# Optimization experiments

Hardware: AMD Instinct MI355X
Metric: run time of the kernel (lower is better)

The kernel has to match this reference:

```python
import jax, jax.numpy as jnp
import numpy as np

B, S, H = 2, 4096, 2048
NH, NKV, D = 16, 4, 128
BS, LOCAL, GLOB, STRIDE = 64, 8, 4, 16
SEL = GLOB + LOCAL
SCALE = D ** -0.5
NEG = -1e9


def rotate_half(x):
    x1, x2 = x[..., : D // 2], x[..., D // 2 :]
    return jnp.concatenate([-x2, x1], axis=-1)


def setup_inputs():
    key = jax.random.key(0)
    ks = jax.random.split(key, 5)
    hidden_states = jax.random.normal(ks[0], (B, S, H), dtype=jnp.float32)
    # standard RoPE tables, shape [B, S, D] as the module expects (cos.unsqueeze(1))
    pos = jnp.arange(S, dtype=jnp.float32)
    inv = 1.0 / (10000.0 ** (jnp.arange(0, D, 2, dtype=jnp.float32) / D))
    freqs = pos[:, None] * inv[None, :]
    emb = jnp.concatenate([freqs, freqs], axis=-1)
    cos = jnp.broadcast_to(jnp.cos(emb)[None], (B, S, D)).astype(jnp.float32)
    sin = jnp.broadcast_to(jnp.sin(emb)[None], (B, S, D)).astype(jnp.float32)
    std = 0.02
    Wq = jax.random.normal(ks[1], (NH * D, H), dtype=jnp.float32) * std
    Wk = jax.random.normal(ks[2], (NKV * D, H), dtype=jnp.float32) * std
    Wv = jax.random.normal(ks[3], (NKV * D, H), dtype=jnp.float32) * std
    Wo = jax.random.normal(ks[4], (H, NH * D), dtype=jnp.float32) * std
    return {"hidden_states": hidden_states, "cos": cos, "sin": sin,
            "Wq": Wq, "Wk": Wk, "Wv": Wv, "Wo": Wo}


def _block_sparse_attn(q, k, v):
    # q, k, v: [B, NH, S, D]; past_len = 0, attention_mask = None (all keys valid)
    qb = S // BS
    kb = S // BS
    qid = jnp.arange(qb)
    # local blocks: the LOCAL most recent blocks ending at the query block
    loc = qid[:, None] - (LOCAL - 1 - jnp.arange(LOCAL)[None, :])
    loc = jnp.clip(loc, 0, kb - 1)
    # global blocks: strided anchors
    g = jnp.clip(jnp.arange(GLOB) * STRIDE, 0, kb - 1)
    glob = jnp.broadcast_to(g[None, :], (qb, GLOB))
    sel = jnp.concatenate([glob, loc], axis=1)  # [qb, SEL]
    valid = sel <= qid[:, None]                 # causal at block level
    # dedup: drop a selected block if an earlier slot selected the same block
    eq = sel[:, :, None] == sel[:, None, :]
    lower = jnp.tril(jnp.ones((SEL, SEL), dtype=bool), k=-1)
    keep = (~(eq & lower[None]).any(-1)) & valid  # [qb, SEL]

    k_blk = k.reshape(B, NH, kb, BS, D)
    v_blk = v.reshape(B, NH, kb, BS, D)
    k_sel = jnp.take(k_blk, sel.reshape(-1), axis=2).reshape(B, NH, qb, SEL * BS, D)
    v_sel = jnp.take(v_blk, sel.reshape(-1), axis=2).reshape(B, NH, qb, SEL * BS, D)
    q_blk = q.reshape(B, NH, qb, BS, D)

    scores = jnp.einsum("bhqid,bhqjd->bhqij", q_blk, k_sel) * SCALE  # [B,NH,qb,BS,SEL*BS]
    keep_tok = jnp.broadcast_to(keep[:, :, None], (qb, SEL, BS)).reshape(qb, SEL * BS)
    scores = scores + (1.0 - keep_tok.astype(scores.dtype))[None, None, :, None, :] * NEG
    # intra-block causal mask where selected block == query block
    same = (sel == qid[:, None]).astype(scores.dtype)  # [qb, SEL]
    intra = jnp.triu(jnp.full((BS, BS), NEG, dtype=scores.dtype), k=1)
    scores6 = scores.reshape(B, NH, qb, BS, SEL, BS)
    scores6 = scores6 + intra[None, None, None, :, None, :] * same[None, None, :, None, :, None]
    scores = scores6.reshape(B, NH, qb, BS, SEL * BS)
    probs = jax.nn.softmax(scores, axis=-1)
    out = jnp.einsum("bhqij,bhqjd->bhqid", probs, v_sel)
    return out.reshape(B, NH, S, D)


def reference(hidden_states, cos, sin, Wq, Wk, Wv, Wo):
    q = (hidden_states @ Wq.T).reshape(B, S, NH, D).transpose(0, 2, 1, 3)
    k = (hidden_states @ Wk.T).reshape(B, S, NKV, D).transpose(0, 2, 1, 3)
    v = (hidden_states @ Wv.T).reshape(B, S, NKV, D).transpose(0, 2, 1, 3)
    c = cos[:, None, :, :]
    s = sin[:, None, :, :]
    q = q * c + rotate_half(q) * s
    k = k * c + rotate_half(k) * s
    rep = NH // NKV
    k = jnp.repeat(k, rep, axis=1)
    v = jnp.repeat(v, rep, axis=1)
    out = _block_sparse_attn(q, k, v)
    out = out.transpose(0, 2, 1, 3).reshape(B, S, NH * D)
    return out @ Wo.T
```

## Files before the change

### kernel.cpp

```cpp
#include <hip/hip_runtime.h>

typedef __bf16 bf16_t;
typedef __bf16 bf16x8_t __attribute__((ext_vector_type(8)));
typedef __bf16 bf16x4_t __attribute__((ext_vector_type(4)));
typedef float f32x4_t __attribute__((ext_vector_type(4)));
typedef unsigned short u16;
typedef unsigned int u32;

#define B_ 2
#define S_ 4096
#define NH_ 16
#define NKV_ 4
#define D_ 128
#define NEG_ (-1000000000.0f)
#define SCALE_ 0.08838834764831845f

__device__ __forceinline__ void load16(const bf16_t* g, bf16_t* l) {
  __builtin_amdgcn_global_load_lds(
      (__attribute__((address_space(1))) void*)(g),
      (__attribute__((address_space(3))) void*)(l),
      16, 0, 0);
}

__global__ __launch_bounds__(256) void cvt_kernel(const float* __restrict__ in,
                                                  bf16_t* __restrict__ out, int n4) {
  int i = blockIdx.x * 256 + threadIdx.x;
  if (i < n4) {
    float4 v = ((const float4*)in)[i];
    bf16x4_t o;
    o.x = (bf16_t)v.x; o.y = (bf16_t)v.y; o.z = (bf16_t)v.z; o.w = (bf16_t)v.w;
    *(bf16x4_t*)(out + (size_t)i * 4) = o;
  }
}

template <int BF16OUT>
__global__ __launch_bounds__(256) void gemm_bt_kernel(const bf16_t* __restrict__ A,
                                                      const bf16_t* __restrict__ Bm,
                                                      float* __restrict__ Cf,
                                                      bf16_t* __restrict__ Cb,
                                                      int M, int N, int K) {
  __shared__ bf16_t As[128 * 32];
  __shared__ bf16_t Bs[128 * 32];
  const int t = threadIdx.x;
  const int lane = t & 63;
  const int w = t >> 6;
  const int wr = w >> 1, wc = w & 1;
  const int l15 = lane & 15, l4 = lane >> 4;
  const int m0 = blockIdx.x * 128;
  const int n0 = blockIdx.y * 128;

  f32x4_t acc[4][4] = {};

  for (int k0 = 0; k0 < K; k0 += 32) {
    __syncthreads();
#pragma unroll
    for (int i = 0; i < 2; i++) {
      int f = t + 256 * i;
      int row = f >> 2, c = f & 3;
      load16(A + (size_t)(m0 + row) * K + k0 + c * 8, As + (w * 64 + i * 256) * 8);
      load16(Bm + (size_t)(n0 + row) * K + k0 + c * 8, Bs + (w * 64 + i * 256) * 8);
    }
    __syncthreads();
    bf16x8_t af[4], bfr[4];
#pragma unroll
    for (int mi = 0; mi < 4; mi++)
      af[mi] = *(const bf16x8_t*)&As[(wr * 64 + mi * 16 + l15) * 32 + l4 * 8];
#pragma unroll
    for (int ni = 0; ni < 4; ni++)
      bfr[ni] = *(const bf16x8_t*)&Bs[(wc * 64 + ni * 16 + l15) * 32 + l4 * 8];
#pragma unroll
    for (int mi = 0; mi < 4; mi++)
#pragma unroll
      for (int ni = 0; ni < 4; ni++)
        acc[mi][ni] = __builtin_amdgcn_mfma_f32_16x16x32_bf16(af[mi], bfr[ni], acc[mi][ni], 0, 0, 0);
  }

#pragma unroll
  for (int mi = 0; mi < 4; mi++)
#pragma unroll
    for (int ni = 0; ni < 4; ni++)
#pragma unroll
      for (int r = 0; r < 4; r++) {
        int grow = m0 + wr * 64 + mi * 16 + l4 * 4 + r;
        int gcol = n0 + wc * 64 + ni * 16 + l15;
        float v = acc[mi][ni][r];
        if (BF16OUT) Cb[(size_t)grow * N + gcol] = (bf16_t)v;
        else Cf[(size_t)grow * N + gcol] = v;
      }
}

__global__ __launch_bounds__(320) void rope_kernel(const bf16_t* __restrict__ qkv,
                                                   const float* __restrict__ cosp,
                                                   const float* __restrict__ sinp,
                                                   bf16_t* __restrict__ Qro,
                                                   bf16_t* __restrict__ Kro) {
  const int tk = blockIdx.x;
  const int b = tk >> 12;
  const int s = tk & 4095;
  const int sblock = s >> 6, row = s & 63;
  const int idx = threadIdx.x;
  int head, lc;
  const bf16_t* base;
  bf16_t* outp;
  if (idx < 256) {
    head = idx >> 4; lc = idx & 15;
    base = qkv + (size_t)tk * 3072 + head * 128;
    outp = Qro + ((size_t)(b * NH_ + head) * 64 + sblock) * 8192;
  } else {
    int i2 = idx - 256;
    head = i2 >> 4; lc = i2 & 15;
    base = qkv + (size_t)tk * 3072 + 2048 + head * 128;
    outp = Kro + ((size_t)(b * NKV_ + head) * 64 + sblock) * 8192;
  }
  const int d0 = lc * 8;
  bf16x8_t x = *(const bf16x8_t*)(base + d0);
  const int d0p = (d0 < 64) ? d0 + 64 : d0 - 64;
  bf16x8_t xp = *(const bf16x8_t*)(base + d0p);
  const float sgn = (d0 < 64) ? -1.0f : 1.0f;
  const float* cb = cosp + (size_t)tk * 128 + d0;
  const float* sb = sinp + (size_t)tk * 128 + d0;
  bf16x8_t o;
#pragma unroll
  for (int e = 0; e < 8; e++)
    o[e] = (bf16_t)((float)x[e] * cb[e] + sgn * (float)xp[e] * sb[e]);
  *(bf16x8_t*)(outp + (lc * 64 + row) * 8) = o;
}

__global__ __launch_bounds__(256) void vtrans_kernel(const u16* __restrict__ qkv,
                                                     u16* __restrict__ vt) {
  __shared__ u16 tile[64][136];
  const int sblock = blockIdx.x;
  const int kh = blockIdx.y;
  const int b = blockIdx.z;
  const int t = threadIdx.x;
#pragma unroll
  for (int i = 0; i < 4; i++) {
    int f = t + 256 * i;
    int sl = f >> 4, c = f & 15;
    uint4 vv = *(const uint4*)(qkv + (size_t)(b * S_ + sblock * 64 + sl) * 3072 + 2560 + kh * 128 + c * 8);
    *(uint4*)&tile[sl][c * 8] = vv;
  }
  __syncthreads();
  u16* out = vt + ((size_t)(b * NKV_ + kh) * 64 + sblock) * 8192;
#pragma unroll
  for (int i = 0; i < 4; i++) {
    int g = t + 256 * i;
    int sc = g >> 7, d = g & 127;
    u16 e0 = tile[sc * 8 + 0][d], e1 = tile[sc * 8 + 1][d];
    u16 e2 = tile[sc * 8 + 2][d], e3 = tile[sc * 8 + 3][d];
    u16 e4 = tile[sc * 8 + 4][d], e5 = tile[sc * 8 + 5][d];
    u16 e6 = tile[sc * 8 + 6][d], e7 = tile[sc * 8 + 7][d];
    uint4 ov;
    ov.x = (u32)e0 | ((u32)e1 << 16);
    ov.y = (u32)e2 | ((u32)e3 << 16);
    ov.z = (u32)e4 | ((u32)e5 << 16);
    ov.w = (u32)e6 | ((u32)e7 << 16);
    *(uint4*)(out + (size_t)g * 8) = ov;
  }
}

__global__ __launch_bounds__(256) void attn_kernel(const bf16_t* __restrict__ Qr,
                                                   const bf16_t* __restrict__ Kr,
                                                   const bf16_t* __restrict__ Vt,
                                                   bf16_t* __restrict__ Ao) {
  __shared__ bf16_t Ks[8192];
  __shared__ bf16_t Vs[8192];
  __shared__ bf16_t Ps[4 * 16 * 72];
  const int qid = blockIdx.x;
  const int h = blockIdx.y;
  const int b = blockIdx.z;
  const int kh = h >> 2;
  const int t = threadIdx.x;
  const int lane = t & 63;
  const int w = t >> 6;
  const int l15 = lane & 15, l4 = lane >> 4;

  int keep_mask = 0;
#pragma unroll
  for (int j = 0; j < 12; j++) {
    int cj;
    if (j < 4) cj = j * 16;
    else { cj = qid - 11 + j; cj = cj < 0 ? 0 : cj; cj = cj > 63 ? 63 : cj; }
    bool keep = (cj <= qid);
#pragma unroll
    for (int i = 0; i < j; i++) {
      int ci;
      if (i < 4) ci = i * 16;
      else { ci = qid - 11 + i; ci = ci < 0 ? 0 : ci; ci = ci > 63 ? 63 : ci; }
      if (ci == cj) keep = false;
    }
    if (keep) keep_mask |= (1 << j);
  }

  const bf16_t* Qg = Qr + ((size_t)(b * NH_ + h) * 64 + qid) * 8192;
  const bf16_t* Kg = Kr + ((size_t)(b * NKV_ + kh) * 64) * 8192;
  const bf16_t* Vg = Vt + ((size_t)(b * NKV_ + kh) * 64) * 8192;

#pragma unroll
  for (int i = 0; i < 4; i++) {
    int f = t + 256 * i;
    load16(Qg + (size_t)f * 8, Ks + (w * 64 + i * 256) * 8);
  }
  __syncthreads();
  bf16x8_t qa[4];
#pragma unroll
  for (int ks = 0; ks < 4; ks++)
    qa[ks] = *(const bf16x8_t*)&Ks[((ks * 4 + l4) * 64 + w * 16 + l15) * 8];

  float mi_r[4], li_r[4];
  f32x4_t oacc[8] = {};
#pragma unroll
  for (int r = 0; r < 4; r++) { mi_r[r] = -__builtin_inff(); li_r[r] = 0.0f; }

#pragma unroll 1
  for (int j = 0; j < 12; j++) {
    if (!(keep_mask & (1 << j))) continue;
    int cj;
    if (j < 4) cj = j * 16;
    else { cj = qid - 11 + j; cj = cj < 0 ? 0 : cj; cj = cj > 63 ? 63 : cj; }

    __syncthreads();
#pragma unroll
    for (int i = 0; i < 4; i++) {
      int f = t + 256 * i;
      load16(Kg + (size_t)cj * 8192 + (size_t)f * 8, Ks + (w * 64 + i * 256) * 8);
      load16(Vg + (size_t)cj * 8192 + (size_t)f * 8, Vs + (w * 64 + i * 256) * 8);
    }
    __syncthreads();

    f32x4_t sacc[4] = {};
#pragma unroll
    for (int ks = 0; ks < 4; ks++) {
#pragma unroll
      for (int ni = 0; ni < 4; ni++) {
        bf16x8_t kb = *(const bf16x8_t*)&Ks[((ks * 4 + l4) * 64 + ni * 16 + l15) * 8];
        sacc[ni] = __builtin_amdgcn_mfma_f32_16x16x32_bf16(qa[ks], kb, sacc[ni], 0, 0, 0);
      }
    }

    const bool diag = (cj == qid);
    float sv[4][4];
#pragma unroll
    for (int ni = 0; ni < 4; ni++)
#pragma unroll
      for (int r = 0; r < 4; r++) {
        float x = sacc[ni][r] * SCALE_;
        if (diag && (ni * 16 + l15) > (w * 16 + l4 * 4 + r)) x += NEG_;
        sv[ni][r] = x;
      }

    float rmax[4], rsum[4], alpha[4], p[4][4];
#pragma unroll
    for (int r = 0; r < 4; r++)
      rmax[r] = fmaxf(fmaxf(sv[0][r], sv[1][r]), fmaxf(sv[2][r], sv[3][r]));
#pragma unroll
    for (int msk = 1; msk < 16; msk <<= 1)
#pragma unroll
      for (int r = 0; r < 4; r++)
        rmax[r] = fmaxf(rmax[r], __shfl_xor(rmax[r], msk, 64));
#pragma unroll
    for (int r = 0; r < 4; r++) {
      float nm = fmaxf(mi_r[r], rmax[r]);
      alpha[r] = __expf(mi_r[r] - nm);
      mi_r[r] = nm;
    }
#pragma unroll
    for (int ni = 0; ni < 4; ni++)
#pragma unroll
      for (int r = 0; r < 4; r++)
        p[ni][r] = __expf(sv[ni][r] - mi_r[r]);
#pragma unroll
    for (int r = 0; r < 4; r++)
      rsum[r] = (p[0][r] + p[1][r]) + (p[2][r] + p[3][r]);
#pragma unroll
    for (int msk = 1; msk < 16; msk <<= 1)
#pragma unroll
      for (int r = 0; r < 4; r++)
        rsum[r] += __shfl_xor(rsum[r], msk, 64);
#pragma unroll
    for (int r = 0; r < 4; r++)
      li_r[r] = li_r[r] * alpha[r] + rsum[r];
#pragma unroll
    for (int n2 = 0; n2 < 8; n2++)
#pragma unroll
      for (int r = 0; r < 4; r++)
        oacc[n2][r] *= alpha[r];

#pragma unroll
    for (int ni = 0; ni < 4; ni++)
#pragma unroll
      for (int r = 0; r < 4; r++)
        Ps[w * 1152 + (l4 * 4 + r) * 72 + ni * 16 + l15] = (bf16_t)p[ni][r];

#pragma unroll
    for (int kst = 0; kst < 2; kst++) {
      bf16x8_t pa = *(const bf16x8_t*)&Ps[w * 1152 + l15 * 72 + kst * 32 + l4 * 8];
#pragma unroll
      for (int n2 = 0; n2 < 8; n2++) {
        bf16x8_t vb = *(const bf16x8_t*)&Vs[((kst * 4 + l4) * 128 + n2 * 16 + l15) * 8];
        oacc[n2] = __builtin_amdgcn_mfma_f32_16x16x32_bf16(pa, vb, oacc[n2], 0, 0, 0);
      }
    }
  }

  float invl[4];
#pragma unroll
  for (int r = 0; r < 4; r++) invl[r] = 1.0f / li_r[r];
#pragma unroll
  for (int n2 = 0; n2 < 8; n2++)
#pragma unroll
    for (int r = 0; r < 4; r++) {
      int m = w * 16 + l4 * 4 + r;
      size_t idx = ((size_t)(b * S_ + qid * 64 + m)) * (NH_ * D_) + h * D_ + n2 * 16 + l15;
      Ao[idx] = (bf16_t)(oacc[n2][r] * invl[r]);
    }
}

extern "C" void kernel_launch(void* const* d_in, const int* in_sizes, int n_in,
                              void* d_out, int out_size, void* d_ws, size_t ws_size,
                              hipStream_t stream) {
  const float* hs = (const float*)d_in[0];
  const float* cosp = (const float*)d_in[1];
  const float* sinp = (const float*)d_in[2];
  const float* Wq = (const float*)d_in[3];
  const float* Wk = (const float*)d_in[4];
  const float* Wv = (const float*)d_in[5];
  const float* Wo = (const float*)d_in[6];
  float* outp = (float*)d_out;

  char* ws = (char*)d_ws;
  bf16_t* Xb   = (bf16_t*)(ws);
  bf16_t* Wb   = (bf16_t*)(ws + 33554432);
  bf16_t* Wob  = (bf16_t*)(ws + 46137344);
  bf16_t* QKVo = (bf16_t*)(ws + 54525952);
  bf16_t* Qr   = (bf16_t*)(ws + 104857600);
  bf16_t* Kr   = (bf16_t*)(ws + 138412032);
  bf16_t* Vt   = (bf16_t*)(ws + 146800640);
  bf16_t* Ao   = QKVo;

  {
    int n4;
    n4 = 16777216 / 4; cvt_kernel<<<dim3((n4 + 255) / 256), dim3(256), 0, stream>>>(hs, Xb, n4);
    n4 = 4194304 / 4;  cvt_kernel<<<dim3((n4 + 255) / 256), dim3(256), 0, stream>>>(Wq, Wb, n4);
    n4 = 1048576 / 4;  cvt_kernel<<<dim3((n4 + 255) / 256), dim3(256), 0, stream>>>(Wk, Wb + 4194304, n4);
    n4 = 1048576 / 4;  cvt_kernel<<<dim3((n4 + 255) / 256), dim3(256), 0, stream>>>(Wv, Wb + 5242880, n4);
    n4 = 4194304 / 4;  cvt_kernel<<<dim3((n4 + 255) / 256), dim3(256), 0, stream>>>(Wo, Wob, n4);
  }

  gemm_bt_kernel<1><<<dim3(64, 24), dim3(256), 0, stream>>>(Xb, Wb, (float*)nullptr, QKVo,
                                                            8192, 3072, 2048);
  rope_kernel<<<dim3(8192), dim3(320), 0, stream>>>(QKVo, cosp, sinp, Qr, Kr);
  vtrans_kernel<<<dim3(64, NKV_, B_), dim3(256), 0, stream>>>((const u16*)QKVo, (u16*)Vt);
  attn_kernel<<<dim3(64, NH_, B_), dim3(256), 0, stream>>>(Qr, Kr, Vt, Ao);
  gemm_bt_kernel<0><<<dim3(64, 16), dim3(256), 0, stream>>>(Ao, Wob, outp, (bf16_t*)nullptr,
                                                            8192, 2048, 2048);
}
```

Baseline: 543.7 us.

## Share KV blocks across GQA heads, fuse conversions, remap GEMM tiles per XCD

The attention kernel now handles all four query heads of a KV group in one 512-thread block. Each wave processes two 16-row tiles, so every K/V block is loaded into LDS once per group instead of once per head. Q fragments are read straight from global memory instead of being staged through LDS. The five fp32-to-bf16 conversion launches become a single launch. GEMM block indices are remapped so that tiles sharing N columns land on the same XCD, which should improve L2 reuse. The trade-offs are fewer attention blocks (512), which may lower occupancy, and higher register pressure.

Result: no change. 540.6 us (-0.6%).

```diff
diff --git a/kernel.cpp b/kernel.cpp
--- a/kernel.cpp
+++ b/kernel.cpp
@@ -22,15 +22,25 @@
       16, 0, 0);
 }
 
-__global__ __launch_bounds__(256) void cvt_kernel(const float* __restrict__ in,
-                                                  bf16_t* __restrict__ out, int n4) {
+__global__ __launch_bounds__(256) void cvt_all_kernel(const float* __restrict__ hs,
+                                                      const float* __restrict__ Wq,
+                                                      const float* __restrict__ Wk,
+                                                      const float* __restrict__ Wv,
+                                                      const float* __restrict__ Wo,
+                                                      bf16_t* __restrict__ Xb,
+                                                      bf16_t* __restrict__ Wb,
+                                                      bf16_t* __restrict__ Wob) {
   int i = blockIdx.x * 256 + threadIdx.x;
-  if (i < n4) {
-    float4 v = ((const float4*)in)[i];
-    bf16x4_t o;
-    o.x = (bf16_t)v.x; o.y = (bf16_t)v.y; o.z = (bf16_t)v.z; o.w = (bf16_t)v.w;
-    *(bf16x4_t*)(out + (size_t)i * 4) = o;
-  }
+  const float* src; bf16_t* dst; int local;
+  if (i < 4194304)      { src = hs; dst = Xb;            local = i; }
+  else if (i < 5242880) { src = Wq; dst = Wb;            local = i - 4194304; }
+  else if (i < 5505024) { src = Wk; dst = Wb + 4194304;  local = i - 5242880; }
+  else if (i < 5767168) { src = Wv; dst = Wb + 5242880;  local = i - 5505024; }
+  else                  { src = Wo; dst = Wob;           local = i - 5767168; }
+  float4 v = ((const float4*)src)[local];
+  bf16x4_t o;
+  o.x = (bf16_t)v.x; o.y = (bf16_t)v.y; o.z = (bf16_t)v.z; o.w = (bf16_t)v.w;
+  *(bf16x4_t*)(dst + (size_t)local * 4) = o;
 }
 
 template <int BF16OUT>
@@ -46,8 +56,11 @@
   const int w = t >> 6;
   const int wr = w >> 1, wc = w & 1;
   const int l15 = lane & 15, l4 = lane >> 4;
-  const int m0 = blockIdx.x * 128;
-  const int n0 = blockIdx.y * 128;
+  const int id = blockIdx.y * 64 + blockIdx.x;
+  const int xcd = id & 7;
+  const int loc = id >> 3;
+  const int m0 = (loc & 63) * 128;
+  const int n0 = (xcd * (gridDim.y >> 3) + (loc >> 6)) * 128;
 
   f32x4_t acc[4][4] = {};
 
@@ -159,21 +172,24 @@
   }
 }
 
-__global__ __launch_bounds__(256) void attn_kernel(const bf16_t* __restrict__ Qr,
+__global__ __launch_bounds__(512) void attn_kernel(const bf16_t* __restrict__ Qr,
                                                    const bf16_t* __restrict__ Kr,
                                                    const bf16_t* __restrict__ Vt,
                                                    bf16_t* __restrict__ Ao) {
   __shared__ bf16_t Ks[8192];
   __shared__ bf16_t Vs[8192];
-  __shared__ bf16_t Ps[4 * 16 * 72];
+  __shared__ bf16_t Ps[16 * 16 * 72];
   const int qid = blockIdx.x;
-  const int h = blockIdx.y;
+  const int kh = blockIdx.y;
   const int b = blockIdx.z;
-  const int kh = h >> 2;
   const int t = threadIdx.x;
   const int lane = t & 63;
   const int w = t >> 6;
   const int l15 = lane & 15, l4 = lane >> 4;
+  const int h = kh * 4 + ((w * 2) >> 2);
+  int row0[2];
+  row0[0] = ((w * 2) & 3) * 16;
+  row0[1] = ((w * 2 + 1) & 3) * 16;
 
   int keep_mask = 0;
 #pragma unroll
@@ -196,21 +212,19 @@
   const bf16_t* Kg = Kr + ((size_t)(b * NKV_ + kh) * 64) * 8192;
   const bf16_t* Vg = Vt + ((size_t)(b * NKV_ + kh) * 64) * 8192;
 
-#pragma unroll
-  for (int i = 0; i < 4; i++) {
-    int f = t + 256 * i;
-    load16(Qg + (size_t)f * 8, Ks + (w * 64 + i * 256) * 8);
-  }
-  __syncthreads();
-  bf16x8_t qa[4];
-#pragma unroll
-  for (int ks = 0; ks < 4; ks++)
-    qa[ks] = *(const bf16x8_t*)&Ks[((ks * 4 + l4) * 64 + w * 16 + l15) * 8];
-
-  float mi_r[4], li_r[4];
-  f32x4_t oacc[8] = {};
-#pragma unroll
-  for (int r = 0; r < 4; r++) { mi_r[r] = -__builtin_inff(); li_r[r] = 0.0f; }
+  bf16x8_t qa[2][4];
+#pragma unroll
+  for (int mt = 0; mt < 2; mt++)
+#pragma unroll
+    for (int ks = 0; ks < 4; ks++)
+      qa[mt][ks] = *(const bf16x8_t*)(Qg + ((ks * 4 + l4) * 64 + row0[mt] + l15) * 8);
+
+  float mi_r[2][4], li_r[2][4];
+  f32x4_t oacc[2][8] = {};
+#pragma unroll
+  for (int mt = 0; mt < 2; mt++)
+#pragma unroll
+    for (int r = 0; r < 4; r++) { mi_r[mt][r] = -__builtin_inff(); li_r[mt][r] = 0.0f; }
 
 #pragma unroll 1
   for (int j = 0; j < 12; j++) {
@@ -221,99 +235,111 @@
 
     __syncthreads();
 #pragma unroll
-    for (int i = 0; i < 4; i++) {
-      int f = t + 256 * i;
-      load16(Kg + (size_t)cj * 8192 + (size_t)f * 8, Ks + (w * 64 + i * 256) * 8);
-      load16(Vg + (size_t)cj * 8192 + (size_t)f * 8, Vs + (w * 64 + i * 256) * 8);
+    for (int i = 0; i < 2; i++) {
+      int f = t + 512 * i;
+      load16(Kg + (size_t)cj * 8192 + (size_t)f * 8, Ks + (w * 64 + i * 512) * 8);
+      load16(Vg + (size_t)cj * 8192 + (size_t)f * 8, Vs + (w * 64 + i * 512) * 8);
     }
     __syncthreads();
 
-    f32x4_t sacc[4] = {};
-#pragma unroll
-    for (int ks = 0; ks < 4; ks++) {
+    f32x4_t sacc[2][4] = {};
+#pragma unroll
+    for (int ks = 0; ks < 4; ks++)
 #pragma unroll
       for (int ni = 0; ni < 4; ni++) {
         bf16x8_t kb = *(const bf16x8_t*)&Ks[((ks * 4 + l4) * 64 + ni * 16 + l15) * 8];
-        sacc[ni] = __builtin_amdgcn_mfma_f32_16x16x32_bf16(qa[ks], kb, sacc[ni], 0, 0, 0);
-      }
-    }
+#pragma unroll
+        for (int mt = 0; mt < 2; mt++)
+          sacc[mt][ni] = __builtin_amdgcn_mfma_f32_16x16x32_bf16(qa[mt][ks], kb, sacc[mt][ni], 0, 0, 0);
+      }
 
     const bool diag = (cj == qid);
-    float sv[4][4];
-#pragma unroll
-    for (int ni = 0; ni < 4; ni++)
+#pragma unroll
+    for (int mt = 0; mt < 2; mt++) {
+      float sv[4][4];
+#pragma unroll
+      for (int ni = 0; ni < 4; ni++)
+#pragma unroll
+        for (int r = 0; r < 4; r++) {
+          float x = sacc[mt][ni][r] * SCALE_;
+          if (diag && (ni * 16 + l15) > (row0[mt] + l4 * 4 + r)) x += NEG_;
+          sv[ni][r] = x;
+        }
+
+      float rmax[4], rsum[4], alpha[4], p[4][4];
+#pragma unroll
+      for (int r = 0; r < 4; r++)
+        rmax[r] = fmaxf(fmaxf(sv[0][r], sv[1][r]), fmaxf(sv[2][r], sv[3][r]));
+#pragma unroll
+      for (int msk = 1; msk < 16; msk <<= 1)
+#pragma unroll
+        for (int r = 0; r < 4; r++)
+          rmax[r] = fmaxf(rmax[r], __shfl_xor(rmax[r], msk, 64));
 #pragma unroll
       for (int r = 0; r < 4; r++) {
-        float x = sacc[ni][r] * SCALE_;
-        if (diag && (ni * 16 + l15) > (w * 16 + l4 * 4 + r)) x += NEG_;
-        sv[ni][r] = x;
-      }
-
-    float rmax[4], rsum[4], alpha[4], p[4][4];
-#pragma unroll
-    for (int r = 0; r < 4; r++)
-      rmax[r] = fmaxf(fmaxf(sv[0][r], sv[1][r]), fmaxf(sv[2][r], sv[3][r]));
-#pragma unroll
-    for (int msk = 1; msk < 16; msk <<= 1)
+        float nm = fmaxf(mi_r[mt][r], rmax[r]);
+        alpha[r] = __expf(mi_r[mt][r] - nm);
+        mi_r[mt][r] = nm;
+      }
+#pragma unroll
+      for (int ni = 0; ni < 4; ni++)
+#pragma unroll
+        for (int r = 0; r < 4; r++)
+          p[ni][r] = __expf(sv[ni][r] - mi_r[mt][r]);
 #pragma unroll
       for (int r = 0; r < 4; r++)
-        rmax[r] = fmaxf(rmax[r], __shfl_xor(rmax[r], msk, 64));
-#pragma unroll
-    for (int r = 0; r < 4; r++) {
-      float nm = fmaxf(mi_r[r], rmax[r]);
-      alpha[r] = __expf(mi_r[r] - nm);
-      mi_r[r] = nm;
-    }
-#pragma unroll
-    for (int ni = 0; ni < 4; ni++)
+        rsum[r] = (p[0][r] + p[1][r]) + (p[2][r] + p[3][r]);
+#pragma unroll
+      for (int msk = 1; msk < 16; msk <<= 1)
+#pragma unroll
+        for (int r = 0; r < 4; r++)
+          rsum[r] += __shfl_xor(rsum[r], msk, 64);
 #pragma unroll
       for (int r = 0; r < 4; r++)
-        p[ni][r] = __expf(sv[ni][r] - mi_r[r]);
-#pragma unroll
-    for (int r = 0; r < 4; r++)
-      rsum[r] = (p[0][r] + p[1][r]) + (p[2][r] + p[3][r]);
-#pragma unroll
-    for (int msk = 1; msk < 16; msk <<= 1)
-#pragma unroll
-      for (int r = 0; r < 4; r++)
-        rsum[r] += __shfl_xor(rsum[r], msk, 64);
-#pragma unroll
-    for (int r = 0; r < 4; r++)
-      li_r[r] = li_r[r] * alpha[r] + rsum[r];
-#pragma unroll
-    for (int n2 = 0; n2 < 8; n2++)
-#pragma unroll
-      for (int r = 0; r < 4; r++)
-        oacc[n2][r] *= alpha[r];
-
-#pragma unroll
-    for (int ni = 0; ni < 4; ni++)
-#pragma unroll
-      for (int r = 0; r < 4; r++)
-        Ps[w * 1152 + (l4 * 4 + r) * 72 + ni * 16 + l15] = (bf16_t)p[ni][r];
+        li_r[mt][r] = li_r[mt][r] * alpha[r] + rsum[r];
+#pragma unroll
+      for (int n2 = 0; n2 < 8; n2++)
+#pragma unroll
+        for (int r = 0; r < 4; r++)
+          oacc[mt][n2][r] *= alpha[r];
+
+#pragma unroll
+      for (int ni = 0; ni < 4; ni++)
+#pragma unroll
+        for (int r = 0; r < 4; r++)
+          Ps[(w * 2 + mt) * 1152 + (l4 * 4 + r) * 72 + ni * 16 + l15] = (bf16_t)p[ni][r];
+    }
 
 #pragma unroll
     for (int kst = 0; kst < 2; kst++) {
-      bf16x8_t pa = *(const bf16x8_t*)&Ps[w * 1152 + l15 * 72 + kst * 32 + l4 * 8];
+      bf16x8_t pa[2];
+#pragma unroll
+      for (int mt = 0; mt < 2; mt++)
+        pa[mt] = *(const bf16x8_t*)&Ps[(w * 2 + mt) * 1152 + l15 * 72 + kst * 32 + l4 * 8];
 #pragma unroll
       for (int n2 = 0; n2 < 8; n2++) {
         bf16x8_t vb = *(const bf16x8_t*)&Vs[((kst * 4 + l4) * 128 + n2 * 16 + l15) * 8];
-        oacc[n2] = __builtin_amdgcn_mfma_f32_16x16x32_bf16(pa, vb, oacc[n2], 0, 0, 0);
-      }
-    }
-  }
-
-  float invl[4];
-#pragma unroll
-  for (int r = 0; r < 4; r++) invl[r] = 1.0f / li_r[r];
-#pragma unroll
-  for (int n2 = 0; n2 < 8; n2++)
-#pragma unroll
-    for (int r = 0; r < 4; r++) {
-      int m = w * 16 + l4 * 4 + r;
-      size_t idx = ((size_t)(b * S_ + qid * 64 + m)) * (NH_ * D_) + h * D_ + n2 * 16 + l15;
-      Ao[idx] = (bf16_t)(oacc[n2][r] * invl[r]);
-    }
+#pragma unroll
+        for (int mt = 0; mt < 2; mt++)
+          oacc[mt][n2] = __builtin_amdgcn_mfma_f32_16x16x32_bf16(pa[mt], vb, oacc[mt][n2], 0, 0, 0);
+      }
+    }
+  }
+
+#pragma unroll
+  for (int mt = 0; mt < 2; mt++) {
+    float invl[4];
+#pragma unroll
+    for (int r = 0; r < 4; r++) invl[r] = 1.0f / li_r[mt][r];
+#pragma unroll
+    for (int n2 = 0; n2 < 8; n2++)
+#pragma unroll
+      for (int r = 0; r < 4; r++) {
+        int m = row0[mt] + l4 * 4 + r;
+        size_t idx = ((size_t)(b * S_ + qid * 64 + m)) * (NH_ * D_) + h * D_ + n2 * 16 + l15;
+        Ao[idx] = (bf16_t)(oacc[mt][n2][r] * invl[r]);
+      }
+  }
 }
 
 extern "C" void kernel_launch(void* const* d_in, const int* in_sizes, int n_in,
@@ -338,20 +364,13 @@
   bf16_t* Vt   = (bf16_t*)(ws + 146800640);
   bf16_t* Ao   = QKVo;
 
-  {
-    int n4;
-    n4 = 16777216 / 4; cvt_kernel<<<dim3((n4 + 255) / 256), dim3(256), 0, stream>>>(hs, Xb, n4);
-    n4 = 4194304 / 4;  cvt_kernel<<<dim3((n4 + 255) / 256), dim3(256), 0, stream>>>(Wq, Wb, n4);
-    n4 = 1048576 / 4;  cvt_kernel<<<dim3((n4 + 255) / 256), dim3(256), 0, stream>>>(Wk, Wb + 4194304, n4);
-    n4 = 1048576 / 4;  cvt_kernel<<<dim3((n4 + 255) / 256), dim3(256), 0, stream>>>(Wv, Wb + 5242880, n4);
-    n4 = 4194304 / 4;  cvt_kernel<<<dim3((n4 + 255) / 256), dim3(256), 0, stream>>>(Wo, Wob, n4);
-  }
+  cvt_all_kernel<<<dim3(26624), dim3(256), 0, stream>>>(hs, Wq, Wk, Wv, Wo, Xb, Wb, Wob);
 
   gemm_bt_kernel<1><<<dim3(64, 24), dim3(256), 0, stream>>>(Xb, Wb, (float*)nullptr, QKVo,
                                                             8192, 3072, 2048);
   rope_kernel<<<dim3(8192), dim3(320), 0, stream>>>(QKVo, cosp, sinp, Qr, Kr);
   vtrans_kernel<<<dim3(64, NKV_, B_), dim3(256), 0, stream>>>((const u16*)QKVo, (u16*)Vt);
-  attn_kernel<<<dim3(64, NH_, B_), dim3(256), 0, stream>>>(Qr, Kr, Vt, Ao);
+  attn_kernel<<<dim3(64, NKV_, B_), dim3(512), 0, stream>>>(Qr, Kr, Vt, Ao);
   gemm_bt_kernel<0><<<dim3(64, 16), dim3(256), 0, stream>>>(Ao, Wob, outp, (bf16_t*)nullptr,
                                                             8192, 2048, 2048);
 }
```
